# Kernel tuning notes

Hardware: AMD Instinct MI355X
Metric: run time of the kernel (lower is better)

## Reference

```python
import jax, jax.numpy as jnp
import numpy as np

B, T, C, H = 4, 2048, 1024, 16
HS = C // H  # head size 64
LN_EPS = 1e-5


def setup_inputs() -> dict:
    key = jax.random.key(0)
    ks = jax.random.split(key, 14)
    s = lambda fan_in: 1.0 / np.sqrt(fan_in)
    return {
        "x": jax.random.normal(ks[0], (B, T, C), jnp.float32),
        # weights stored [in, out] (transposed vs torch nn.Linear) for y = x @ W + b
        "c_attn_w": jax.random.normal(ks[1], (C, 3 * C), jnp.float32) * s(C),
        "c_attn_b": jnp.zeros((3 * C,), jnp.float32),
        "c_proj_w": jax.random.normal(ks[2], (C, C), jnp.float32) * s(C),
        "c_proj_b": jnp.zeros((C,), jnp.float32),
        "fc_w": jax.random.normal(ks[3], (C, 4 * C), jnp.float32) * s(C),
        "fc_b": jnp.zeros((4 * C,), jnp.float32),
        "proj_w": jax.random.normal(ks[4], (4 * C, C), jnp.float32) * s(4 * C),
        "proj_b": jnp.zeros((C,), jnp.float32),
        "ln1_g": jnp.ones((C,), jnp.float32),
        "ln1_b": jnp.zeros((C,), jnp.float32),
        "ln2_g": jnp.ones((C,), jnp.float32),
        "ln2_b": jnp.zeros((C,), jnp.float32),
    }


def layer_norm(x, g, b):
    mu = jnp.mean(x, axis=-1, keepdims=True)
    var = jnp.var(x, axis=-1, keepdims=True)
    return (x - mu) * jax.lax.rsqrt(var + LN_EPS) * g + b


def attention(x, c_attn_w, c_attn_b, c_proj_w, c_proj_b):
    Bs, Ts, Cs = x.shape
    qkv = x @ c_attn_w + c_attn_b  # (B,T,3C)
    q, k, v = jnp.split(qkv, 3, axis=-1)
    q = q.reshape(Bs, Ts, H, HS).transpose(0, 2, 1, 3)  # (B,H,T,hs)
    k = k.reshape(Bs, Ts, H, HS).transpose(0, 2, 1, 3)
    v = v.reshape(Bs, Ts, H, HS).transpose(0, 2, 1, 3)
    wei = jnp.einsum("bhqd,bhkd->bhqk", q, k) * (1.0 / np.sqrt(HS))
    causal = jnp.tril(jnp.ones((Ts, Ts), bool))
    wei = jnp.where(causal, wei, -jnp.inf)
    wei = jax.nn.softmax(wei, axis=-1)
    out = jnp.einsum("bhqk,bhkd->bhqd", wei, v)
    out = out.transpose(0, 2, 1, 3).reshape(Bs, Ts, Cs)
    return out @ c_proj_w + c_proj_b


def mlp(x, fc_w, fc_b, proj_w, proj_b):
    h = jax.nn.gelu(x @ fc_w + fc_b, approximate=True)
    return h @ proj_w + proj_b


def reference(x, c_attn_w, c_attn_b, c_proj_w, c_proj_b, fc_w, fc_b, proj_w, proj_b, ln1_g, ln1_b, ln2_g, ln2_b):
    x = x + attention(layer_norm(x, ln1_g, ln1_b), c_attn_w, c_attn_b, c_proj_w, c_proj_b)
    out = x + mlp(layer_norm(x, ln2_g, ln2_b), fc_w, fc_b, proj_w, proj_b)
    return out
```

## Files before the change

### kernel.cpp

```cpp
#include <hip/hip_runtime.h>

typedef unsigned short u16;
typedef __attribute__((ext_vector_type(8))) short bf16x8;
typedef __attribute__((ext_vector_type(4))) float f32x4;

#define SC_LOG2E 0.18033688011112043f
#define MB_LOG2E 17.31234049066756f

__device__ __forceinline__ float b2f(u16 u) {
  union { unsigned int i; float f; } v; v.i = ((unsigned int)u) << 16; return v.f;
}
__device__ __forceinline__ u16 f2b(float f) {
  unsigned int x = __float_as_uint(f);
  unsigned int r = (x + 0x7fffu + ((x >> 16) & 1u)) >> 16;
  return (u16)r;
}

#define GLOAD_LDS16(g, l)                                                              \
  __builtin_amdgcn_global_load_lds((const __attribute__((address_space(1))) void*)(g), \
                                   (__attribute__((address_space(3))) void*)(l), 16, 0, 0)

struct TJob { const float* in; u16* out; int K, N, nbx, nblocks; };

__global__ __launch_bounds__(256) void prep_kernel(TJob j0, TJob j1, TJob j2, TJob j3,
                                                   const float* __restrict__ xv,
                                                   const float* __restrict__ g,
                                                   const float* __restrict__ bb,
                                                   u16* __restrict__ o) {
  const int tid = threadIdx.x;
  if (blockIdx.x < 3072) {
    int bid = blockIdx.x;
    TJob j = j0;
    if (bid >= j.nblocks) { bid -= j.nblocks; j = j1; }
    if (bid >= j.nblocks) { bid -= j.nblocks; j = j2; }
    if (bid >= j.nblocks) { bid -= j.nblocks; j = j3; }
    const int n0 = (bid % j.nbx) * 64, k0 = (bid / j.nbx) * 64;
    const int N = j.N, K = j.K;
    const float* __restrict__ in = j.in;
    u16* __restrict__ out = j.out;

    __shared__ float tile[64][65];
#pragma unroll
    for (int it = 0; it < 4; ++it) {
      int lin = it * 256 + tid;
      int r = lin >> 4, c4 = (lin & 15) * 4;
      float4 v = *(const float4*)&in[(size_t)(k0 + r) * N + n0 + c4];
      tile[r][c4 + 0] = v.x; tile[r][c4 + 1] = v.y;
      tile[r][c4 + 2] = v.z; tile[r][c4 + 3] = v.w;
    }
    __syncthreads();
#pragma unroll
    for (int it = 0; it < 2; ++it) {
      int lin = it * 256 + tid;
      int r = lin >> 3, c8 = (lin & 7) * 8;
      u16 tmp[8];
#pragma unroll
      for (int jj = 0; jj < 8; ++jj) tmp[jj] = f2b(tile[c8 + jj][r]);
      *(uint4*)&out[(size_t)(n0 + r) * K + k0 + c8] = *(const uint4*)tmp;
    }
  } else {
    const int row = blockIdx.x - 3072;
    const int wave = tid >> 6, lane = tid & 63;
    const int base = tid * 4;
    float4 v = *(const float4*)&xv[(size_t)row * 1024 + base];
    float f[4] = {v.x, v.y, v.z, v.w};
    float s = f[0] + f[1] + f[2] + f[3];
    float q = f[0] * f[0] + f[1] * f[1] + f[2] * f[2] + f[3] * f[3];
#pragma unroll
    for (int off = 1; off < 64; off <<= 1) {
      s += __shfl_xor(s, off);
      q += __shfl_xor(q, off);
    }
    __shared__ float reds[4], redq[4];
    if (lane == 0) { reds[wave] = s; redq[wave] = q; }
    __syncthreads();
    float S = reds[0] + reds[1] + reds[2] + reds[3];
    float Q = redq[0] + redq[1] + redq[2] + redq[3];
    const float inv = 1.0f / 1024.0f;
    float mean = S * inv;
    float var = Q * inv - mean * mean;
    float rs = rsqrtf(var + 1e-5f);
    float4 gv = *(const float4*)&g[base];
    float4 bv = *(const float4*)&bb[base];
    ushort4 ov;
    ov.x = f2b((f[0] - mean) * rs * gv.x + bv.x);
    ov.y = f2b((f[1] - mean) * rs * gv.y + bv.y);
    ov.z = f2b((f[2] - mean) * rs * gv.z + bv.z);
    ov.w = f2b((f[3] - mean) * rs * gv.w + bv.w);
    *(ushort4*)&o[(size_t)row * 1024 + base] = ov;
  }
}

__global__ __launch_bounds__(256) void ln_kernel(const u16* __restrict__ xv,
                                                 const float* __restrict__ g,
                                                 const float* __restrict__ b,
                                                 u16* __restrict__ o) {
  const int row = blockIdx.x, tid = threadIdx.x;
  const int wave = tid >> 6, lane = tid & 63;
  const int base = tid * 4;
  ushort4 v = *(const ushort4*)&xv[(size_t)row * 1024 + base];
  float f[4] = {b2f(v.x), b2f(v.y), b2f(v.z), b2f(v.w)};
  float s = f[0] + f[1] + f[2] + f[3];
  float q = f[0] * f[0] + f[1] * f[1] + f[2] * f[2] + f[3] * f[3];
#pragma unroll
  for (int off = 1; off < 64; off <<= 1) {
    s += __shfl_xor(s, off);
    q += __shfl_xor(q, off);
  }
  __shared__ float reds[4], redq[4];
  if (lane == 0) { reds[wave] = s; redq[wave] = q; }
  __syncthreads();
  float S = reds[0] + reds[1] + reds[2] + reds[3];
  float Q = redq[0] + redq[1] + redq[2] + redq[3];
  const float inv = 1.0f / 1024.0f;
  float mean = S * inv;
  float var = Q * inv - mean * mean;
  float rs = rsqrtf(var + 1e-5f);
  float4 gv = *(const float4*)&g[base];
  float4 bv = *(const float4*)&b[base];
  ushort4 ov;
  ov.x = f2b((f[0] - mean) * rs * gv.x + bv.x);
  ov.y = f2b((f[1] - mean) * rs * gv.y + bv.y);
  ov.z = f2b((f[2] - mean) * rs * gv.z + bv.z);
  ov.w = f2b((f[3] - mean) * rs * gv.w + bv.w);
  *(ushort4*)&o[(size_t)row * 1024 + base] = ov;
}

__device__ __forceinline__ float gelu_fn(float v) {
  float a = 0.7978845608028654f * __builtin_fmaf(0.044715f * v * v, v, v);
  float t = __builtin_amdgcn_exp2f(a * -2.8853900817779268f);
  return v * __builtin_amdgcn_rcpf(1.0f + t);
}

template <bool GELU, int RESMODE, bool OUTF32, bool VSPLIT>
__global__ __launch_bounds__(512, 4) void gemm8_kernel(const u16* __restrict__ A,
                                                       const u16* __restrict__ Bt,
                                                       const float* __restrict__ bias,
                                                       const void* __restrict__ res,
                                                       void* __restrict__ Cv,
                                                       u16* __restrict__ vt,
                                                       int M, int N, int K) {
  __shared__ u16 As[128 * 64];
  __shared__ u16 Bs[128 * 64];
  const int tid = threadIdx.x;
  const int wave = tid >> 6, lane = tid & 63;
  const int lhi = lane >> 4, llo = lane & 15;
  const int sw = llo & 7;
  const int m0 = blockIdx.x * 128, n0 = blockIdx.y * 128;
  const int wr = (wave & 3) * 32, wc = (wave >> 2) * 64;

  f32x4 acc[2][4] = {};

  for (int k0 = 0; k0 < K; k0 += 64) {
#pragma unroll
    for (int p = 0; p < 2; ++p) {
      int s = p * 512 + tid;
      int r = s >> 3;
      int c = ((s & 7) ^ (r & 7)) * 8;
      GLOAD_LDS16(A + (size_t)(m0 + r) * K + k0 + c, As + s * 8);
      GLOAD_LDS16(Bt + (size_t)(n0 + r) * K + k0 + c, Bs + s * 8);
    }
    __syncthreads();
#pragma unroll
    for (int kk = 0; kk < 2; ++kk) {
      const int cp = ((kk * 4 + lhi) ^ sw) * 8;
      bf16x8 af[2], bf[4];
#pragma unroll
      for (int i = 0; i < 2; ++i)
        af[i] = *(const bf16x8*)&As[(wr + i * 16 + llo) * 64 + cp];
#pragma unroll
      for (int j = 0; j < 4; ++j)
        bf[j] = *(const bf16x8*)&Bs[(wc + j * 16 + llo) * 64 + cp];
#pragma unroll
      for (int i = 0; i < 2; ++i)
#pragma unroll
        for (int j = 0; j < 4; ++j)
          acc[i][j] = __builtin_amdgcn_mfma_f32_16x16x32_bf16(af[i], bf[j], acc[i][j], 0, 0, 0);
    }
    __syncthreads();
  }

  const bool vblock = VSPLIT && (n0 >= 2048);
#pragma unroll
  for (int i = 0; i < 2; ++i) {
    int row = m0 + wr + i * 16 + lhi * 4;
#pragma unroll
    for (int j = 0; j < 4; ++j) {
      int col = n0 + wc + j * 16 + llo;
      float bv = bias[col];
      if (vblock) {
        const int hcol = col - 2048;
        const int bh = (row >> 11) * 16 + (hcol >> 6);
        const int d = hcol & 63;
        const int t = row & 2047;
        ushort4 tv;
        tv.x = f2b(acc[i][j][0] + bv);
        tv.y = f2b(acc[i][j][1] + bv);
        tv.z = f2b(acc[i][j][2] + bv);
        tv.w = f2b(acc[i][j][3] + bv);
        *(ushort4*)&vt[((size_t)bh * 64 + d) * 2048 + t] = tv;
        continue;
      }
#pragma unroll
      for (int r = 0; r < 4; ++r) {
        float v = acc[i][j][r] + bv;
        if (GELU) v = gelu_fn(v);
        size_t idx = (size_t)(row + r) * N + col;
        if (RESMODE == 1) v += b2f(((const u16*)res)[idx]);
        if (RESMODE == 2) v += ((const float*)res)[idx];
        if (OUTF32) ((float*)Cv)[idx] = v;
        else ((u16*)Cv)[idx] = f2b(v);
      }
    }
  }
}

__global__ __launch_bounds__(512, 4) void attn_kernel(const u16* __restrict__ qkv,
                                                      const u16* __restrict__ vt,
                                                      u16* __restrict__ out) {
  __shared__ u16 Ks[64 * 68];
  __shared__ u16 Vs[64 * 68];
  __shared__ u16 Ps[128 * 68];
  const int tid = threadIdx.x;
  const int wave = tid >> 6, lane = tid & 63;
  const int lhi = lane >> 4, llo = lane & 15;
  const int pr = blockIdx.x;
  const int bh = blockIdx.y;
  const int b = bh >> 4, h = bh & 15;
  const size_t rowbase = (size_t)b * 2048;
  const int qoff = h * 64, koff = 1024 + h * 64;
  const u16* vtb = vt + (size_t)bh * 64 * 2048;
  const int sr = tid >> 3;
  const int sc = (tid & 7) * 8;

#pragma unroll
  for (int ph = 0; ph < 2; ++ph) {
    const int qtile = ph ? pr : (15 - pr);
    const int q0 = qtile * 128;
    const int qrow = q0 + wave * 16;

    bf16x8 qf[2];
#pragma unroll
    for (int kk = 0; kk < 2; ++kk) {
      uint4 v = *(const uint4*)&qkv[(rowbase + qrow + llo) * 3072 + qoff + kk * 32 + lhi * 8];
      qf[kk] = *(const bf16x8*)&v;
    }

    f32x4 oacc[4] = {};
    float l_st[4] = {};
    const int nkt = 2 * qtile + 2;

    uint4 pk = *(const uint4*)&qkv[(rowbase + sr) * 3072 + koff + sc];
    uint4 pv = *(const uint4*)&vtb[(size_t)sr * 2048 + sc];

    for (int kt = 0; kt < nkt; ++kt) {
      const int kt0 = kt * 64;
      __syncthreads();
      *(uint4*)&Ks[sr * 68 + sc] = pk;
      *(uint4*)&Vs[sr * 68 + sc] = pv;
      __syncthreads();
      if (kt + 1 < nkt) {
        const int nt0 = kt0 + 64;
        pk = *(const uint4*)&qkv[(rowbase + nt0 + sr) * 3072 + koff + sc];
        pv = *(const uint4*)&vtb[(size_t)sr * 2048 + nt0 + sc];
      }

      if (kt0 > qrow + 15) continue;

      f32x4 s[4] = {};
#pragma unroll
      for (int kk = 0; kk < 2; ++kk)
#pragma unroll
        for (int j = 0; j < 4; ++j) {
          bf16x8 kf = *(const bf16x8*)&Ks[(j * 16 + llo) * 68 + kk * 32 + lhi * 8];
          s[j] = __builtin_amdgcn_mfma_f32_16x16x32_bf16(qf[kk], kf, s[j], 0, 0, 0);
        }

      const bool msk = (kt0 + 63 > qrow);
      u16* psrow = &Ps[(wave * 16) * 68];
#pragma unroll
      for (int j = 0; j < 4; ++j) {
        const int key = kt0 + j * 16 + llo;
#pragma unroll
        for (int r = 0; r < 4; ++r) {
          float sv = s[j][r];
          if (msk) sv = (key <= qrow + lhi * 4 + r) ? sv : -1e30f;
          float p = __builtin_amdgcn_exp2f(__builtin_fmaf(sv, SC_LOG2E, -MB_LOG2E));
          l_st[r] += p;
          psrow[(lhi * 4 + r) * 68 + j * 16 + llo] = (u16)(__float_as_uint(p) >> 16);
        }
      }

#pragma unroll
      for (int kc = 0; kc < 2; ++kc) {
        bf16x8 pf = *(const bf16x8*)&Ps[(wave * 16 + llo) * 68 + kc * 32 + lhi * 8];
#pragma unroll
        for (int j4 = 0; j4 < 4; ++j4) {
          bf16x8 vf = *(const bf16x8*)&Vs[(j4 * 16 + llo) * 68 + kc * 32 + lhi * 8];
          oacc[j4] = __builtin_amdgcn_mfma_f32_16x16x32_bf16(pf, vf, oacc[j4], 0, 0, 0);
        }
      }
    }

#pragma unroll
    for (int r = 0; r < 4; ++r) {
      float v = l_st[r];
      v += __shfl_xor(v, 1);
      v += __shfl_xor(v, 2);
      v += __shfl_xor(v, 4);
      v += __shfl_xor(v, 8);
      l_st[r] = 1.0f / v;
    }
#pragma unroll
    for (int j4 = 0; j4 < 4; ++j4)
#pragma unroll
      for (int r = 0; r < 4; ++r) {
        size_t row = rowbase + qrow + lhi * 4 + r;
        out[row * 1024 + h * 64 + j4 * 16 + llo] = f2b(oacc[j4][r] * l_st[r]);
      }
  }
}

extern "C" void kernel_launch(void* const* d_in, const int* in_sizes, int n_in,
                              void* d_out, int out_size, void* d_ws, size_t ws_size,
                              hipStream_t stream) {
  const float* x        = (const float*)d_in[0];
  const float* c_attn_w = (const float*)d_in[1];
  const float* c_attn_b = (const float*)d_in[2];
  const float* c_proj_w = (const float*)d_in[3];
  const float* c_proj_b = (const float*)d_in[4];
  const float* fc_w     = (const float*)d_in[5];
  const float* fc_b     = (const float*)d_in[6];
  const float* proj_w   = (const float*)d_in[7];
  const float* proj_b   = (const float*)d_in[8];
  const float* ln1_g    = (const float*)d_in[9];
  const float* ln1_b    = (const float*)d_in[10];
  const float* ln2_g    = (const float*)d_in[11];
  const float* ln2_b    = (const float*)d_in[12];
  float* out = (float*)d_out;
  u16* ws = (u16*)d_ws;

  const size_t M = 8192;
  u16* ln_buf = ws;
  u16* qkv    = ln_buf + M * 1024;
  u16* x1     = qkv + M * 3072;
  u16* hbuf   = x1 + M * 1024;
  u16* wT_a   = hbuf + M * 4096;
  u16* wT_p   = wT_a + 3072 * 1024;
  u16* wT_f   = wT_p + 1024 * 1024;
  u16* wT_m   = wT_f + 4096 * 1024;
  u16* vt     = hbuf;

  TJob ja = {c_attn_w, wT_a, 1024, 3072, 48, 48 * 16};
  TJob jp = {c_proj_w, wT_p, 1024, 1024, 16, 16 * 16};
  TJob jf = {fc_w,     wT_f, 1024, 4096, 64, 64 * 16};
  TJob jm = {proj_w,   wT_m, 4096, 1024, 16, 16 * 64};
  prep_kernel<<<dim3(3072 + 8192), dim3(256), 0, stream>>>(ja, jp, jf, jm, x, ln1_g, ln1_b, ln_buf);

  gemm8_kernel<false, 0, false, true><<<dim3(64, 24), dim3(512), 0, stream>>>(ln_buf, wT_a, c_attn_b, nullptr, qkv, vt, 8192, 3072, 1024);
  attn_kernel<<<dim3(8, 64), dim3(512), 0, stream>>>(qkv, vt, ln_buf);
  gemm8_kernel<false, 2, false, false><<<dim3(64, 8), dim3(512), 0, stream>>>(ln_buf, wT_p, c_proj_b, x, x1, nullptr, 8192, 1024, 1024);
  ln_kernel<<<8192, dim3(256), 0, stream>>>(x1, ln2_g, ln2_b, ln_buf);
  gemm8_kernel<true, 0, false, false><<<dim3(64, 32), dim3(512), 0, stream>>>(ln_buf, wT_f, fc_b, nullptr, hbuf, nullptr, 8192, 4096, 1024);
  gemm8_kernel<false, 1, true, false><<<dim3(64, 8), dim3(512), 0, stream>>>(hbuf, wT_m, proj_b, x1, out, nullptr, 8192, 1024, 4096);
}
```

Before: 455.6 us.

## Double-buffer K/V tiles in attention and raise wave priority around MFMA

```diff
diff --git a/kernel.cpp b/kernel.cpp
--- a/kernel.cpp
+++ b/kernel.cpp
@@ -218,8 +218,8 @@
 __global__ __launch_bounds__(512, 4) void attn_kernel(const u16* __restrict__ qkv,
                                                       const u16* __restrict__ vt,
                                                       u16* __restrict__ out) {
-  __shared__ u16 Ks[64 * 68];
-  __shared__ u16 Vs[64 * 68];
+  __shared__ u16 Ks[2][64 * 68];
+  __shared__ u16 Vs[2][64 * 68];
   __shared__ u16 Ps[128 * 68];
   const int tid = threadIdx.x;
   const int wave = tid >> 6, lane = tid & 63;
@@ -250,56 +250,73 @@
     float l_st[4] = {};
     const int nkt = 2 * qtile + 2;
 
-    uint4 pk = *(const uint4*)&qkv[(rowbase + sr) * 3072 + koff + sc];
-    uint4 pv = *(const uint4*)&vtb[(size_t)sr * 2048 + sc];
+    {
+      uint4 k0 = *(const uint4*)&qkv[(rowbase + sr) * 3072 + koff + sc];
+      uint4 v0 = *(const uint4*)&vtb[(size_t)sr * 2048 + sc];
+      *(uint4*)&Ks[0][sr * 68 + sc] = k0;
+      *(uint4*)&Vs[0][sr * 68 + sc] = v0;
+    }
+    uint4 pk, pv;
+    if (nkt > 1) {
+      pk = *(const uint4*)&qkv[(rowbase + 64 + sr) * 3072 + koff + sc];
+      pv = *(const uint4*)&vtb[(size_t)sr * 2048 + 64 + sc];
+    }
+    __syncthreads();
 
     for (int kt = 0; kt < nkt; ++kt) {
       const int kt0 = kt * 64;
+      const int cur = kt & 1;
+      if (kt + 1 < nkt) {
+        *(uint4*)&Ks[cur ^ 1][sr * 68 + sc] = pk;
+        *(uint4*)&Vs[cur ^ 1][sr * 68 + sc] = pv;
+        if (kt + 2 < nkt) {
+          const int nt0 = kt0 + 128;
+          pk = *(const uint4*)&qkv[(rowbase + nt0 + sr) * 3072 + koff + sc];
+          pv = *(const uint4*)&vtb[(size_t)sr * 2048 + nt0 + sc];
+        }
+      }
+
+      if (kt0 <= qrow + 15) {
+        f32x4 s[4] = {};
+        __builtin_amdgcn_s_setprio(1);
+#pragma unroll
+        for (int kk = 0; kk < 2; ++kk)
+#pragma unroll
+          for (int j = 0; j < 4; ++j) {
+            bf16x8 kf = *(const bf16x8*)&Ks[cur][(j * 16 + llo) * 68 + kk * 32 + lhi * 8];
+            s[j] = __builtin_amdgcn_mfma_f32_16x16x32_bf16(qf[kk], kf, s[j], 0, 0, 0);
+          }
+        __builtin_amdgcn_s_setprio(0);
+
+        const bool msk = (kt0 + 63 > qrow);
+        u16* psrow = &Ps[(wave * 16) * 68];
+#pragma unroll
+        for (int j = 0; j < 4; ++j) {
+          const int key = kt0 + j * 16 + llo;
+#pragma unroll
+          for (int r = 0; r < 4; ++r) {
+            float sv = s[j][r];
+            if (msk) sv = (key <= qrow + lhi * 4 + r) ? sv : -1e30f;
+            float p = __builtin_amdgcn_exp2f(__builtin_fmaf(sv, SC_LOG2E, -MB_LOG2E));
+            l_st[r] += p;
+            psrow[(lhi * 4 + r) * 68 + j * 16 + llo] = (u16)(__float_as_uint(p) >> 16);
+          }
+        }
+
+        __builtin_amdgcn_s_setprio(1);
+#pragma unroll
+        for (int kc = 0; kc < 2; ++kc) {
+          bf16x8 pf = *(const bf16x8*)&Ps[(wave * 16 + llo) * 68 + kc * 32 + lhi * 8];
+#pragma unroll
+          for (int j4 = 0; j4 < 4; ++j4) {
+            bf16x8 vf = *(const bf16x8*)&Vs[cur][(j4 * 16 + llo) * 68 + kc * 32 + lhi * 8];
+            oacc[j4] = __builtin_amdgcn_mfma_f32_16x16x32_bf16(pf, vf, oacc[j4], 0, 0, 0);
+          }
+        }
+        __builtin_amdgcn_s_setprio(0);
+      }
+
       __syncthreads();
-      *(uint4*)&Ks[sr * 68 + sc] = pk;
-      *(uint4*)&Vs[sr * 68 + sc] = pv;
-      __syncthreads();
-      if (kt + 1 < nkt) {
-        const int nt0 = kt0 + 64;
-        pk = *(const uint4*)&qkv[(rowbase + nt0 + sr) * 3072 + koff + sc];
-        pv = *(const uint4*)&vtb[(size_t)sr * 2048 + nt0 + sc];
-      }
-
-      if (kt0 > qrow + 15) continue;
-
-      f32x4 s[4] = {};
-#pragma unroll
-      for (int kk = 0; kk < 2; ++kk)
-#pragma unroll
-        for (int j = 0; j < 4; ++j) {
-          bf16x8 kf = *(const bf16x8*)&Ks[(j * 16 + llo) * 68 + kk * 32 + lhi * 8];
-          s[j] = __builtin_amdgcn_mfma_f32_16x16x32_bf16(qf[kk], kf, s[j], 0, 0, 0);
-        }
-
-      const bool msk = (kt0 + 63 > qrow);
-      u16* psrow = &Ps[(wave * 16) * 68];
-#pragma unroll
-      for (int j = 0; j < 4; ++j) {
-        const int key = kt0 + j * 16 + llo;
-#pragma unroll
-        for (int r = 0; r < 4; ++r) {
-          float sv = s[j][r];
-          if (msk) sv = (key <= qrow + lhi * 4 + r) ? sv : -1e30f;
-          float p = __builtin_amdgcn_exp2f(__builtin_fmaf(sv, SC_LOG2E, -MB_LOG2E));
-          l_st[r] += p;
-          psrow[(lhi * 4 + r) * 68 + j * 16 + llo] = (u16)(__float_as_uint(p) >> 16);
-        }
-      }
-
-#pragma unroll
-      for (int kc = 0; kc < 2; ++kc) {
-        bf16x8 pf = *(const bf16x8*)&Ps[(wave * 16 + llo) * 68 + kc * 32 + lhi * 8];
-#pragma unroll
-        for (int j4 = 0; j4 < 4; ++j4) {
-          bf16x8 vf = *(const bf16x8*)&Vs[(j4 * 16 + llo) * 68 + kc * 32 + lhi * 8];
-          oacc[j4] = __builtin_amdgcn_mfma_f32_16x16x32_bf16(pf, vf, oacc[j4], 0, 0, 0);
-        }
-      }
     }
 
 #pragma unroll
```

Result: no change. 459.3 us (+0.8%).
